# Kernel tuning notes

Hardware: AMD Instinct MI355X
Metric: run time of the kernel (lower is better)

## Reference

```python
import jax, jax.numpy as jnp
import numpy as np
import math

L, D, H, B, NT = 4, 512, 8, 128, 512
D_HID = int(D * 4.0 / 3.0)  # 682; linear0 outputs 2*D_HID for reglu
EPS = 1e-5


def layer_norm(x, g, b):
    mu = jnp.mean(x, axis=-1, keepdims=True)
    var = jnp.var(x, axis=-1, keepdims=True)
    return (x - mu) * jax.lax.rsqrt(var + EPS) * g + b


def mha(x_q, x_kv, Wq, bq, Wk, bk, Wv, bv, Wo, bo):
    q = x_q @ Wq.T + bq
    k = x_kv @ Wk.T + bk
    v = x_kv @ Wv.T + bv
    Bq, Sq, _ = q.shape
    Sk = k.shape[1]
    dh = D // H
    q = q.reshape(Bq, Sq, H, dh).transpose(0, 2, 1, 3)  # [B,H,Sq,dh]
    k = k.reshape(Bq, Sk, H, dh).transpose(0, 2, 1, 3)
    v = v.reshape(Bq, Sk, H, dh).transpose(0, 2, 1, 3)
    dots = jnp.einsum('bhqd,bhkd->bhqk', q, k) / math.sqrt(dh)
    attn = jax.nn.softmax(dots, axis=-1)
    o = jnp.einsum('bhqk,bhkd->bhqd', attn, v)
    o = o.transpose(0, 2, 1, 3).reshape(Bq, Sq, D)
    return o @ Wo.T + bo


def reglu(x):
    a, b = jnp.split(x, 2, axis=-1)
    return a * jax.nn.relu(b)


def setup_inputs() -> dict:
    key = jax.random.key(0)
    ks = iter(jax.random.split(key, 32))
    s = 0.02
    return {
        'x_num': jax.random.normal(next(ks), (B, NT, D), jnp.float32),
        'cls_w': jax.random.normal(next(ks), (1, D), jnp.float32) * s,
        'Wq': jax.random.normal(next(ks), (L, D, D), jnp.float32) * s,
        'bq': jnp.zeros((L, D), jnp.float32),
        'Wk': jax.random.normal(next(ks), (L, D, D), jnp.float32) * s,
        'bk': jnp.zeros((L, D), jnp.float32),
        'Wv': jax.random.normal(next(ks), (L, D, D), jnp.float32) * s,
        'bv': jnp.zeros((L, D), jnp.float32),
        'Wo': jax.random.normal(next(ks), (L, D, D), jnp.float32) * s,
        'bo': jnp.zeros((L, D), jnp.float32),
        'l0_w': jax.random.normal(next(ks), (L, 2 * D_HID, D), jnp.float32) * s,
        'l0_b': jnp.zeros((L, 2 * D_HID), jnp.float32),
        'l1_w': jax.random.normal(next(ks), (L, D, D_HID), jnp.float32) * s,
        'l1_b': jnp.zeros((L, D), jnp.float32),
        'n0_g': jnp.ones((L - 1, D), jnp.float32),
        'n0_b': jnp.zeros((L - 1, D), jnp.float32),
        'n1_g': jnp.ones((L, D), jnp.float32),
        'n1_b': jnp.zeros((L, D), jnp.float32),
        'ln_g': jnp.ones((D,), jnp.float32),
        'ln_b': jnp.zeros((D,), jnp.float32),
        'head_w': jax.random.normal(next(ks), (1, D), jnp.float32) * s,
        'head_b': jnp.zeros((1,), jnp.float32),
    }


def reference(x_num, cls_w, Wq, bq, Wk, bk, Wv, bv, Wo, bo,
              l0_w, l0_b, l1_w, l1_b, n0_g, n0_b, n1_g, n1_b,
              ln_g, ln_b, head_w, head_b):
    # prepend CLS token: cls_weight broadcast over batch
    x_cls = jnp.broadcast_to(cls_w[None], (x_num.shape[0], 1, D))
    x = jnp.concatenate([x_cls, x_num], axis=1)  # [B, NT+1, D]
    for i in range(L):
        is_last = i + 1 == L
        # attention block (prenormalization; layer 0 has no norm0)
        xr = layer_norm(x, n0_g[i - 1], n0_b[i - 1]) if i > 0 else x
        x_q = xr[:, :1] if is_last else xr  # last layer: query only CLS
        xr = mha(x_q, xr, Wq[i], bq[i], Wk[i], bk[i], Wv[i], bv[i], Wo[i], bo[i])
        if is_last:
            x = x[:, :1]
        x = x + xr
        # FFN block with reglu
        xr = layer_norm(x, n1_g[i], n1_b[i])
        xr = reglu(xr @ l0_w[i].T + l0_b[i])
        xr = xr @ l1_w[i].T + l1_b[i]
        x = x + xr
    x = x[:, 0]  # CLS representation [B, D]
    x = layer_norm(x, ln_g, ln_b)
    x = jax.nn.relu(x)
    x = x @ head_w.T + head_b
    return x.squeeze(-1)  # [B]
```

## Files before the change

### kernel.cpp

```cpp
#include <hip/hip_runtime.h>
#include <stdint.h>

typedef __attribute__((ext_vector_type(4))) float f32x4;
typedef __attribute__((ext_vector_type(8))) short short8;
typedef __attribute__((ext_vector_type(8))) _Float16 half8;

#define DMODEL 512
#define SEQ 513
#define BATCH 128
#define NROWS (BATCH*SEQ)
#define DHID 682
#define DHID2 1364
#define HP 768
#define QKVS 1536
#define KVB 64
#define NKT 9
#define QSF 0.1803368801111244f

__device__ __forceinline__ float h2f(ushort u){ return (float)__builtin_bit_cast(_Float16, u); }
__device__ __forceinline__ ushort f2h(float f){ return __builtin_bit_cast(ushort, (_Float16)f); }
__device__ __forceinline__ uint pk2h(float a, float b){
  return __builtin_bit_cast(uint, __builtin_amdgcn_cvt_pkrtz(a, b));
}
__device__ __forceinline__ void gload16(const void* g, void* lds){
  __builtin_amdgcn_global_load_lds((const __attribute__((address_space(1))) void*)g,
                                   (__attribute__((address_space(3))) void*)lds, 16, 0, 0);
}
__device__ __forceinline__ int xcd_wg(int orig, int nwg){
  const int q = nwg >> 3, r = nwg & 7;
  const int xcd = orig & 7, idx = orig >> 3;
  return (xcd < r) ? (xcd*(q+1) + idx) : (r*(q+1) + (xcd-r)*q + idx);
}

template<int EPI>
__global__ __launch_bounds__(256,3) void gemm_bt(
    const ushort* __restrict__ A, const ushort* __restrict__ W,
    const float* __restrict__ bias, ushort* __restrict__ Cb, float* __restrict__ Cf,
    int K, int ldc, int gx, int nwg)
{
  __shared__ char lds[32768];
  const int t = threadIdx.x, lane = t & 63, w = t >> 6;
  const int fr = lane & 15, g = lane >> 4;
  const int l7 = lane & 7, l8 = lane >> 3;
  const int wg = xcd_wg(blockIdx.x, nwg);
  const int row0 = (wg / gx) << 7;
  const int col0 = (wg % gx) << 7;
  const int wr = (w >> 1) << 6, wc = (w & 1) << 6;

  const int chunkoff = (l7 ^ l8) << 3;
  const ushort* Ag = A + (size_t)(row0 + w*8 + l8) * K + chunkoff;
  const ushort* Wg = W + (size_t)(col0 + w*8 + l8) * K + chunkoff;

  f32x4 acc[4][4] = {};

  for (int k0 = 0; k0 < K; k0 += 64) {
    __syncthreads();
#pragma unroll
    for (int p = 0; p < 4; ++p) {
      gload16(Ag + (size_t)(p*32)*K + k0, lds + p*4096 + w*1024);
      gload16(Wg + (size_t)(p*32)*K + k0, lds + 16384 + p*4096 + w*1024);
    }
    __syncthreads();
#pragma unroll
    for (int ks = 0; ks < 2; ++ks) {
      half8 af[4], wf[4];
#pragma unroll
      for (int m = 0; m < 4; ++m) {
        const int row = wr + m*16 + fr;
        af[m] = *(const half8*)(lds + row*128 + (((g + ks*4) ^ (fr & 7)) << 4));
      }
#pragma unroll
      for (int n = 0; n < 4; ++n) {
        const int row = wc + n*16 + fr;
        wf[n] = *(const half8*)(lds + 16384 + row*128 + (((g + ks*4) ^ (fr & 7)) << 4));
      }
#pragma unroll
      for (int m = 0; m < 4; ++m)
#pragma unroll
        for (int n = 0; n < 4; ++n)
          acc[m][n] = __builtin_amdgcn_mfma_f32_16x16x32_f16(af[m], wf[n], acc[m][n], 0, 0, 0);
    }
  }

  const int r0 = (lane >> 4) << 2;
#pragma unroll
  for (int m = 0; m < 4; ++m) {
    const int rg = row0 + wr + m*16 + r0;
#pragma unroll
    for (int n = 0; n < 4; ++n) {
      const int cg = col0 + wc + n*16 + fr;
      const float bi = bias[cg];
      if (EPI == 0) {
#pragma unroll
        for (int r = 0; r < 4; ++r)
          Cb[(size_t)(rg + r)*ldc + cg] = f2h(acc[m][n][r] + bi);
      } else {
#pragma unroll
        for (int r = 0; r < 4; ++r) {
          const size_t ix = (size_t)(rg + r)*ldc + cg;
          Cf[ix] += acc[m][n][r] + bi;
        }
      }
    }
  }
}

__global__ __launch_bounds__(256,2) void gemm_ffn(
    const ushort* __restrict__ A, const ushort* __restrict__ Wa, const ushort* __restrict__ Wb,
    const float* __restrict__ ba, const float* __restrict__ bb, ushort* __restrict__ H,
    int K, int ldc, int gx, int nwg)
{
  __shared__ char lds[49152];
  const int t = threadIdx.x, lane = t & 63, w = t >> 6;
  const int fr = lane & 15, g = lane >> 4;
  const int l7 = lane & 7, l8 = lane >> 3;
  const int wg = xcd_wg(blockIdx.x, nwg);
  const int row0 = (wg / gx) << 7;
  const int col0 = (wg % gx) << 7;
  const int wr = (w >> 1) << 6, wc = (w & 1) << 6;

  const int chunkoff = (l7 ^ l8) << 3;
  const ushort* Ag  = A  + (size_t)(row0 + w*8 + l8) * K + chunkoff;
  const ushort* WaG = Wa + (size_t)(col0 + w*8 + l8) * K + chunkoff;
  const ushort* WbG = Wb + (size_t)(col0 + w*8 + l8) * K + chunkoff;

  f32x4 aa[4][4] = {}, ab[4][4] = {};

  for (int k0 = 0; k0 < K; k0 += 64) {
    __syncthreads();
#pragma unroll
    for (int p = 0; p < 4; ++p) {
      gload16(Ag  + (size_t)(p*32)*K + k0, lds + p*4096 + w*1024);
      gload16(WaG + (size_t)(p*32)*K + k0, lds + 16384 + p*4096 + w*1024);
      gload16(WbG + (size_t)(p*32)*K + k0, lds + 32768 + p*4096 + w*1024);
    }
    __syncthreads();
#pragma unroll
    for (int ks = 0; ks < 2; ++ks) {
      half8 af[4], wa[4], wb[4];
#pragma unroll
      for (int m = 0; m < 4; ++m) {
        const int row = wr + m*16 + fr;
        af[m] = *(const half8*)(lds + row*128 + (((g + ks*4) ^ (fr & 7)) << 4));
      }
#pragma unroll
      for (int n = 0; n < 4; ++n) {
        const int row = wc + n*16 + fr;
        const int off = row*128 + (((g + ks*4) ^ (fr & 7)) << 4);
        wa[n] = *(const half8*)(lds + 16384 + off);
        wb[n] = *(const half8*)(lds + 32768 + off);
      }
#pragma unroll
      for (int m = 0; m < 4; ++m)
#pragma unroll
        for (int n = 0; n < 4; ++n) {
          aa[m][n] = __builtin_amdgcn_mfma_f32_16x16x32_f16(af[m], wa[n], aa[m][n], 0, 0, 0);
          ab[m][n] = __builtin_amdgcn_mfma_f32_16x16x32_f16(af[m], wb[n], ab[m][n], 0, 0, 0);
        }
    }
  }

  const int r0 = (lane >> 4) << 2;
#pragma unroll
  for (int m = 0; m < 4; ++m) {
    const int rg = row0 + wr + m*16 + r0;
#pragma unroll
    for (int n = 0; n < 4; ++n) {
      const int cg = col0 + wc + n*16 + fr;
      const float bav = ba[cg], bbv = bb[cg];
#pragma unroll
      for (int r = 0; r < 4; ++r) {
        const float av = aa[m][n][r] + bav;
        const float bv = ab[m][n][r] + bbv;
        H[(size_t)(rg + r)*ldc + cg] = f2h(av * fmaxf(bv, 0.f));
      }
    }
  }
}

__global__ __launch_bounds__(256,4) void attn_flash(
    const ushort* __restrict__ qkv, ushort* __restrict__ o)
{
  const int bid = blockIdx.x;
  const int sw = (bid & 7)*512 + (bid >> 3);
  const int qt = sw & 3;
  const int hb = sw >> 2;
  const int h = hb & 7, b = hb >> 3;
  const int t = threadIdx.x, lane = t & 63, w = t >> 6;
  const int fr = lane & 15, g = lane >> 4, gq4 = g << 2;
  const size_t rowB = (size_t)b * SEQ;
  const ushort* q = qkv;
  const ushort* k = qkv + 512;
  const ushort* v = qkv + 1024;

  __shared__ char lds[40960];
  char* const Ks  = lds;
  char* const Vs  = lds + 8192;
  char* const VTs = lds + 16384;
  char* const pb  = lds + 24576 + w*4096;

  const int qr0 = qt*128 + w*32;

  half8 qf[2][2];
#pragma unroll
  for (int nq = 0; nq < 2; ++nq) {
    const int qrow = qr0 + nq*16 + fr;
#pragma unroll
    for (int kk = 0; kk < 2; ++kk)
      qf[nq][kk] = *(const half8*)&q[(rowB + qrow)*QKVS + h*64 + kk*32 + g*8];
  }

  f32x4 accO[2][4] = {};
  float mrun[2] = {-1e30f, -1e30f};
  float lrun[2] = {0.f, 0.f};

  const int l8 = lane >> 3, l7 = lane & 7;
  const int chunk = l7 ^ l8;
  auto STAGE = [&](int kt2) {
#pragma unroll
    for (int i = 0; i < 2; ++i) {
      const int row = i*32 + (w<<3) + l8;
      const int keyg = min(kt2*KVB + row, 512);
      const size_t gsrc = (rowB + keyg)*QKVS + h*64 + chunk*8;
      gload16(k + gsrc, Ks + i*4096 + w*1024);
      gload16(v + gsrc, Vs + i*4096 + w*1024);
    }
  };

  const int db  = (lane & 7) | ((w & 1) << 3);
  const int kbq = l8 | ((w & 2) << 2);
  const int d0 = db << 2, key0 = kbq << 2;

  STAGE(0);

  for (int kt = 0; kt < NKT; ++kt) {
    __syncthreads();

    f32x4 sc[4][2] = {};
    __builtin_amdgcn_s_setprio(1);
#pragma unroll
    for (int kk = 0; kk < 2; ++kk) {
      half8 kf[4];
#pragma unroll
      for (int mk = 0; mk < 4; ++mk) {
        const int row = mk*16 + fr;
        kf[mk] = *(const half8*)(Ks + row*128 + ((kk*64 + g*16) ^ ((fr&7)<<4)));
      }
#pragma unroll
      for (int mk = 0; mk < 4; ++mk)
#pragma unroll
        for (int nq = 0; nq < 2; ++nq)
          sc[mk][nq] = __builtin_amdgcn_mfma_f32_16x16x32_f16(kf[mk], qf[nq][kk], sc[mk][nq], 0, 0, 0);
    }
    __builtin_amdgcn_s_setprio(0);

    {
      uint2 a[4];
#pragma unroll
      for (int i = 0; i < 4; ++i) {
        const int row = key0 + i;
        a[i] = *(const uint2*)(Vs + row*128 + ((d0*2) ^ ((row&7)<<4)));
      }
      uint2 bb[4];
      bb[0].x = (a[0].x & 0xffffu) | (a[1].x << 16);
      bb[0].y = (a[2].x & 0xffffu) | (a[3].x << 16);
      bb[1].x = (a[0].x >> 16) | (a[1].x & 0xffff0000u);
      bb[1].y = (a[2].x >> 16) | (a[3].x & 0xffff0000u);
      bb[2].x = (a[0].y & 0xffffu) | (a[1].y << 16);
      bb[2].y = (a[2].y & 0xffffu) | (a[3].y << 16);
      bb[3].x = (a[0].y >> 16) | (a[1].y & 0xffff0000u);
      bb[3].y = (a[2].y >> 16) | (a[3].y & 0xffff0000u);
#pragma unroll
      for (int j = 0; j < 4; ++j) {
        const int drow = d0 + j;
        *(uint2*)(VTs + drow*128 + ((key0*2) ^ ((drow&7)<<4))) = bb[j];
      }
    }

    if (kt == NKT-1) {
#pragma unroll
      for (int mk = 0; mk < 4; ++mk)
#pragma unroll
        for (int r = 0; r < 4; ++r)
          if (mk + gq4 + r) { sc[mk][0][r] = -1e30f; sc[mk][1][r] = -1e30f; }
    }

    __syncthreads();

    if (kt+1 < NKT) STAGE(kt+1);

    float al2[2];
    bool resc[2];
#pragma unroll
    for (int nq = 0; nq < 2; ++nq) {
      float tm = sc[0][nq][0];
#pragma unroll
      for (int mk = 0; mk < 4; ++mk)
#pragma unroll
        for (int r = 0; r < 4; ++r) tm = fmaxf(tm, sc[mk][nq][r]);
      tm = fmaxf(tm, __shfl_xor(tm, 16));
      tm = fmaxf(tm, __shfl_xor(tm, 32));
      float mref;
      if (__all(tm - mrun[nq] <= 8.f)) {
        mref = mrun[nq];
        al2[nq] = 1.f; resc[nq] = false;
      } else {
        const float mnew = fmaxf(mrun[nq], tm);
        al2[nq] = exp2f(mrun[nq] - mnew);
        mrun[nq] = mnew;
        mref = mnew;
        resc[nq] = true;
      }
      float rs = 0.f;
#pragma unroll
      for (int mk = 0; mk < 4; ++mk)
#pragma unroll
        for (int r = 0; r < 4; ++r) {
          const float pv = exp2f(sc[mk][nq][r] - mref);
          sc[mk][nq][r] = pv;
          rs += pv;
        }
      rs += __shfl_xor(rs, 16);
      rs += __shfl_xor(rs, 32);
      lrun[nq] = resc[nq] ? (lrun[nq]*al2[nq] + rs) : (lrun[nq] + rs);
      char* prow = pb + (nq*16 + fr)*128;
#pragma unroll
      for (int mk = 0; mk < 4; ++mk) {
        uint2 pk;
        pk.x = pk2h(sc[mk][nq][0], sc[mk][nq][1]);
        pk.y = pk2h(sc[mk][nq][2], sc[mk][nq][3]);
        *(uint2*)(prow + ((mk*32 + gq4*2) ^ ((fr&7)<<4))) = pk;
      }
    }

#pragma unroll
    for (int mq = 0; mq < 2; ++mq) {
      if (resc[mq]) {
#pragma unroll
        for (int r = 0; r < 4; ++r) {
          const float alr = __shfl(al2[mq], (lane & 48) | (gq4 + r));
#pragma unroll
          for (int dn = 0; dn < 4; ++dn) accO[mq][dn][r] *= alr;
        }
      }
    }

    asm volatile("" ::: "memory");

    __builtin_amdgcn_s_setprio(1);
#pragma unroll
    for (int kk2 = 0; kk2 < 2; ++kk2) {
      half8 pf[2];
#pragma unroll
      for (int mq = 0; mq < 2; ++mq)
        pf[mq] = *(const half8*)(pb + (mq*16 + fr)*128 + ((kk2*64 + g*16) ^ ((fr&7)<<4)));
      half8 vf[4];
#pragma unroll
      for (int dn = 0; dn < 4; ++dn) {
        const int row = dn*16 + fr;
        vf[dn] = *(const half8*)(VTs + row*128 + ((kk2*64 + g*16) ^ ((fr&7)<<4)));
      }
#pragma unroll
      for (int mq = 0; mq < 2; ++mq)
#pragma unroll
        for (int dn = 0; dn < 4; ++dn)
          accO[mq][dn] = __builtin_amdgcn_mfma_f32_16x16x32_f16(pf[mq], vf[dn], accO[mq][dn], 0, 0, 0);
    }
    __builtin_amdgcn_s_setprio(0);
  }

#pragma unroll
  for (int mq = 0; mq < 2; ++mq)
#pragma unroll
    for (int r = 0; r < 4; ++r) {
      const int qrow = qr0 + mq*16 + gq4 + r;
      const float ls = __shfl(lrun[mq], (lane & 48) | (gq4 + r));
      const float inv = 1.f / ls;
#pragma unroll
      for (int dn = 0; dn < 4; ++dn)
        o[(rowB + qrow)*DMODEL + h*64 + dn*16 + fr] = f2h(accO[mq][dn][r] * inv);
    }
}

__global__ __launch_bounds__(256) void attn_cls(
    const ushort* __restrict__ qbase, size_t qstride,
    const ushort* __restrict__ qkv,
    ushort* __restrict__ obase, size_t ostride)
{
  const int bh = blockIdx.x;
  const int b = bh >> 3, h = bh & 7;
  const int t = threadIdx.x;
  __shared__ float sc[SEQ];
  __shared__ float qsh[64];
  __shared__ float red[8];
  __shared__ float osum[256];
  const ushort* k = qkv + 512;
  const ushort* v = qkv + 1024;
  if (t < 64) qsh[t] = h2f(qbase[(size_t)b*qstride + h*64 + t]);
  __syncthreads();
  for (int key = t; key < SEQ; key += 256) {
    const ushort* kr = k + ((size_t)b*SEQ + key)*QKVS + h*64;
    float s = 0.f;
#pragma unroll 8
    for (int d = 0; d < 64; ++d) s += qsh[d]*h2f(kr[d]);
    sc[key] = s;
  }
  __syncthreads();
  float lm = -1e30f;
  for (int key = t; key < SEQ; key += 256) lm = fmaxf(lm, sc[key]);
#pragma unroll
  for (int mask=1; mask<64; mask<<=1) lm = fmaxf(lm, __shfl_xor(lm, mask));
  if ((t&63)==0) red[t>>6] = lm;
  __syncthreads();
  const float mx = fmaxf(fmaxf(red[0],red[1]), fmaxf(red[2],red[3]));
  float ls = 0.f;
  for (int key = t; key < SEQ; key += 256){ float pp = exp2f(sc[key]-mx); sc[key]=pp; ls += pp; }
#pragma unroll
  for (int mask=1; mask<64; mask<<=1) ls += __shfl_xor(ls, mask);
  if ((t&63)==0) red[4 + (t>>6)] = ls;
  __syncthreads();
  const float ssum = red[4]+red[5]+red[6]+red[7];
  const int d = t & 63, kc = t >> 6;
  float op = 0.f;
  for (int key = kc; key < SEQ; key += 4)
    op += sc[key] * h2f(v[((size_t)b*SEQ + key)*QKVS + h*64 + d]);
  osum[t] = op;
  __syncthreads();
  if (t < 64) {
    const float oo = (osum[t]+osum[64+t]+osum[128+t]+osum[192+t]) / ssum;
    obase[(size_t)b*ostride + h*64 + t] = f2h(oo);
  }
}

__global__ __launch_bounds__(256) void ln_kernel(
    const float* __restrict__ x, const float* __restrict__ gamma, const float* __restrict__ beta,
    ushort* __restrict__ out, int nrows)
{
  const int row = blockIdx.x*4 + (threadIdx.x >> 6);
  const int lane = threadIdx.x & 63;
  if (row >= nrows) return;
  const float* xr = x + (size_t)row*DMODEL;
  float4 a = *(const float4*)(xr + lane*8);
  float4 b = *(const float4*)(xr + lane*8 + 4);
  float s  = a.x+a.y+a.z+a.w+b.x+b.y+b.z+b.w;
  float ss = a.x*a.x+a.y*a.y+a.z*a.z+a.w*a.w+b.x*b.x+b.y*b.y+b.z*b.z+b.w*b.w;
#pragma unroll
  for (int mask=1; mask<64; mask<<=1){ s += __shfl_xor(s,mask); ss += __shfl_xor(ss,mask); }
  const float mu = s*(1.f/512.f);
  const float rstd = rsqrtf(ss*(1.f/512.f) - mu*mu + 1e-5f);
  float vals[8] = {a.x,a.y,a.z,a.w,b.x,b.y,b.z,b.w};
  short8 pk;
#pragma unroll
  for (int j=0;j<8;++j){
    const int c = lane*8 + j;
    pk[j] = (short)f2h((vals[j]-mu)*rstd*gamma[c] + beta[c]);
  }
  *(short8*)(out + (size_t)row*DMODEL + lane*8) = pk;
}

__global__ void embed_kernel(const float* __restrict__ x_num, const float* __restrict__ cls_w,
                             float* __restrict__ x, ushort* __restrict__ xb)
{
  const size_t i = (size_t)blockIdx.x*256 + threadIdx.x;
  if (i >= (size_t)NROWS*128) return;
  const int row = (int)(i >> 7);
  const int c4 = ((int)(i & 127)) << 2;
  const int b = row / SEQ;
  const int s = row - b*SEQ;
  float4 val;
  if (s == 0) val = *(const float4*)(cls_w + c4);
  else        val = *(const float4*)(x_num + ((size_t)b*512 + (s-1))*512 + c4);
  *(float4*)(x + (size_t)row*DMODEL + c4) = val;
  ushort4 pk;
  pk.x = f2h(val.x); pk.y = f2h(val.y); pk.z = f2h(val.z); pk.w = f2h(val.w);
  *(ushort4*)(xb + (size_t)row*DMODEL + c4) = pk;
}

__global__ void convert_pad(const float* __restrict__ in, ushort* __restrict__ out,
                            int R, int C, int RP, int CP, int layers, float scale,
                            int r0, int srcRL, size_t ostride)
{
  const size_t i = (size_t)blockIdx.x*256 + threadIdx.x;
  const size_t per = (size_t)RP*CP;
  if (i >= per*layers) return;
  const int l = (int)(i / per);
  const int rem = (int)(i - (size_t)l*per);
  const int r = rem / CP;
  const int c = rem - r*CP;
  ushort val = 0;
  if (r < R && c < C) val = f2h(in[((size_t)l*srcRL + r0 + r)*C + c] * scale);
  out[(size_t)l*ostride + (size_t)r*CP + c] = val;
}

__global__ void build_bias(const float* __restrict__ bq, const float* __restrict__ bk,
                           const float* __restrict__ bv, const float* __restrict__ l0b,
                           float* __restrict__ fqkv, float* __restrict__ fa, float* __restrict__ fb)
{
  const int i = blockIdx.x*256 + threadIdx.x;
  if (i < 4*1536) {
    const int l = i / 1536, j = i - l*1536;
    float val;
    if (j < 512)       val = bq[l*512 + j] * QSF;
    else if (j < 1024) val = bk[l*512 + j - 512];
    else               val = bv[l*512 + j - 1024];
    fqkv[i] = val;
  }
  if (i < 4*HP) {
    const int l = i / HP, j = i - l*HP;
    fa[i] = (j < DHID) ? l0b[l*DHID2 + j] : 0.f;
    fb[i] = (j < DHID) ? l0b[l*DHID2 + DHID + j] : 0.f;
  }
}

__global__ void gather_cls(const ushort* __restrict__ xb, const float* __restrict__ x,
                           ushort* __restrict__ xq, float* __restrict__ xc)
{
  const int b = blockIdx.x, lane = threadIdx.x;
  const size_t src = (size_t)b*SEQ*DMODEL;
  *(short8*)(xq + b*DMODEL + lane*8) = *(const short8*)(xb + src + lane*8);
  *(float4*)(xc + b*DMODEL + lane*8)     = *(const float4*)(x + src + lane*8);
  *(float4*)(xc + b*DMODEL + lane*8 + 4) = *(const float4*)(x + src + lane*8 + 4);
}

__global__ void head_kernel(const float* __restrict__ xc, const float* __restrict__ g,
                            const float* __restrict__ be, const float* __restrict__ hw,
                            const float* __restrict__ hb, float* __restrict__ out)
{
  const int row = blockIdx.x;
  const int lane = threadIdx.x;
  const float* xr = xc + (size_t)row*DMODEL;
  float4 a = *(const float4*)(xr + lane*8);
  float4 b = *(const float4*)(xr + lane*8 + 4);
  float s  = a.x+a.y+a.z+a.w+b.x+b.y+b.z+b.w;
  float ss = a.x*a.x+a.y*a.y+a.z*a.z+a.w*a.w+b.x*b.x+b.y*b.y+b.z*b.z+b.w*b.w;
#pragma unroll
  for (int mask=1; mask<64; mask<<=1){ s += __shfl_xor(s,mask); ss += __shfl_xor(ss,mask); }
  const float mu = s*(1.f/512.f);
  const float rstd = rsqrtf(ss*(1.f/512.f) - mu*mu + 1e-5f);
  float vals[8] = {a.x,a.y,a.z,a.w,b.x,b.y,b.z,b.w};
  float acc = 0.f;
#pragma unroll
  for (int j=0;j<8;++j){
    const int c = lane*8 + j;
    float tv = (vals[j]-mu)*rstd*g[c] + be[c];
    acc += fmaxf(tv, 0.f) * hw[c];
  }
#pragma unroll
  for (int mask=1; mask<64; mask<<=1) acc += __shfl_xor(acc, mask);
  if (lane==0) out[row] = acc + hb[0];
}

extern "C" void kernel_launch(void* const* d_in, const int* in_sizes, int n_in,
                              void* d_out, int out_size, void* d_ws, size_t ws_size,
                              hipStream_t stream)
{
  const float* x_num = (const float*)d_in[0];
  const float* cls_w = (const float*)d_in[1];
  const float* Wq = (const float*)d_in[2];
  const float* bq = (const float*)d_in[3];
  const float* Wk = (const float*)d_in[4];
  const float* bk = (const float*)d_in[5];
  const float* Wv = (const float*)d_in[6];
  const float* bv = (const float*)d_in[7];
  const float* Wo = (const float*)d_in[8];
  const float* bo = (const float*)d_in[9];
  const float* l0_w = (const float*)d_in[10];
  const float* l0_b = (const float*)d_in[11];
  const float* l1_w = (const float*)d_in[12];
  const float* l1_b = (const float*)d_in[13];
  const float* n0_g = (const float*)d_in[14];
  const float* n0_b = (const float*)d_in[15];
  const float* n1_g = (const float*)d_in[16];
  const float* n1_b = (const float*)d_in[17];
  const float* ln_g = (const float*)d_in[18];
  const float* ln_b = (const float*)d_in[19];
  const float* head_w = (const float*)d_in[20];
  const float* head_b = (const float*)d_in[21];
  float* out = (float*)d_out;

  char* p = (char*)d_ws;
  auto alloc = [&](size_t bytes){ char* r = p; p += (bytes + 255) & ~(size_t)255; return r; };

  float* x  = (float*)alloc((size_t)NROWS*DMODEL*4);
  char* U   = alloc((size_t)NROWS*DMODEL*2);
  ushort* xb = (ushort*)U;
  ushort* ob = (ushort*)U;
  char* QKVG = alloc((size_t)NROWS*QKVS*2);
  ushort* qkv = (ushort*)QKVG;
  ushort* hbuf = (ushort*)QKVG;
  ushort* wqkvb = (ushort*)alloc((size_t)4*QKVS*512*2);
  ushort* wob  = (ushort*)alloc((size_t)4*512*512*2);
  ushort* wl0a = (ushort*)alloc((size_t)4*HP*512*2);
  ushort* wl0b = (ushort*)alloc((size_t)4*HP*512*2);
  ushort* l1wp = (ushort*)alloc((size_t)4*512*HP*2);
  float*  fqkvb = (float*)alloc((size_t)4*QKVS*4);
  float*  l0ba = (float*)alloc((size_t)4*HP*4);
  float*  l0bb = (float*)alloc((size_t)4*HP*4);
  ushort* xq_cls = (ushort*)alloc(128*512*2);
  float*  xcf = (float*)alloc(128*512*4);
  ushort* qc = (ushort*)alloc(128*512*2);
  ushort* oc = (ushort*)alloc(128*512*2);
  ushort* hc = (ushort*)alloc((size_t)128*HP*2);
  ushort* xcb = (ushort*)alloc(128*512*2);

  auto cdiv = [](size_t a, size_t b){ return (unsigned)((a + b - 1)/b); };

  convert_pad<<<cdiv((size_t)4*512*512,256),256,0,stream>>>(Wq, wqkvb,            512,512,512,512,4, QSF, 0, 512, (size_t)QKVS*512);
  convert_pad<<<cdiv((size_t)4*512*512,256),256,0,stream>>>(Wk, wqkvb + 512*512,  512,512,512,512,4, 1.f, 0, 512, (size_t)QKVS*512);
  convert_pad<<<cdiv((size_t)4*512*512,256),256,0,stream>>>(Wv, wqkvb + 1024*512, 512,512,512,512,4, 1.f, 0, 512, (size_t)QKVS*512);
  convert_pad<<<cdiv((size_t)4*512*512,256),256,0,stream>>>(Wo, wob, 512,512,512,512,4, 1.f, 0, 512, (size_t)512*512);
  convert_pad<<<cdiv((size_t)4*HP*512,256),256,0,stream>>>(l0_w, wl0a, DHID,512,HP,512,4, 1.f, 0,    DHID2, (size_t)HP*512);
  convert_pad<<<cdiv((size_t)4*HP*512,256),256,0,stream>>>(l0_w, wl0b, DHID,512,HP,512,4, 1.f, DHID, DHID2, (size_t)HP*512);
  convert_pad<<<cdiv((size_t)4*512*HP,256),256,0,stream>>>(l1_w, l1wp, 512,DHID,512,HP,4, 1.f, 0, 512, (size_t)512*HP);
  build_bias<<<cdiv(4*QKVS,256),256,0,stream>>>(bq, bk, bv, l0_b, fqkvb, l0ba, l0bb);

  embed_kernel<<<cdiv((size_t)NROWS*128,256),256,0,stream>>>(x_num, cls_w, x, xb);

  const int nwQKV = 12*513, nwO = 4*513, nwF = 6*513, nwL1 = 4*513, nwKV = 8*513;
  for (int i = 0; i < 3; ++i) {
    if (i > 0)
      ln_kernel<<<cdiv(NROWS,4),256,0,stream>>>(x, n0_g+(size_t)(i-1)*512, n0_b+(size_t)(i-1)*512, xb, NROWS);
    gemm_bt<0><<<nwQKV,256,0,stream>>>(xb, wqkvb+(size_t)i*QKVS*512, fqkvb+(size_t)i*QKVS, qkv, nullptr, 512, QKVS, 12, nwQKV);
    attn_flash<<<4096,256,0,stream>>>(qkv, ob);
    attn_cls<<<1024,256,0,stream>>>(qkv + (size_t)512*QKVS, (size_t)SEQ*QKVS, qkv,
                                    ob + (size_t)512*DMODEL, (size_t)SEQ*DMODEL);
    gemm_bt<1><<<nwO,256,0,stream>>>(ob, wob+(size_t)i*262144, bo+i*512, nullptr, x, 512, 512, 4, nwO);
    ln_kernel<<<cdiv(NROWS,4),256,0,stream>>>(x, n1_g+(size_t)i*512, n1_b+(size_t)i*512, xb, NROWS);
    gemm_ffn<<<nwF,256,0,stream>>>(xb, wl0a+(size_t)i*HP*512, wl0b+(size_t)i*HP*512,
                                   l0ba+(size_t)i*HP, l0bb+(size_t)i*HP, hbuf, 512, HP, 6, nwF);
    gemm_bt<1><<<nwL1,256,0,stream>>>(hbuf, l1wp+(size_t)i*512*HP, l1_b+i*512, nullptr, x, HP, 512, 4, nwL1);
  }

  ln_kernel<<<cdiv(NROWS,4),256,0,stream>>>(x, n0_g+2*512, n0_b+2*512, xb, NROWS);
  gather_cls<<<128,64,0,stream>>>(xb, x, xq_cls, xcf);
  gemm_bt<0><<<4,256,0,stream>>>(xq_cls, wqkvb+(size_t)3*QKVS*512, fqkvb+(size_t)3*QKVS, qc, nullptr, 512, 512, 4, 4);
  gemm_bt<0><<<nwKV,256,0,stream>>>(xb, wqkvb+(size_t)3*QKVS*512 + 512*512, fqkvb+(size_t)3*QKVS + 512,
                                    qkv + 512, nullptr, 512, QKVS, 8, nwKV);
  attn_cls<<<1024,256,0,stream>>>(qc, 512, qkv, oc, 512);
  gemm_bt<1><<<4,256,0,stream>>>(oc, wob+(size_t)3*262144, bo+3*512, nullptr, xcf, 512, 512, 4, 4);
  ln_kernel<<<cdiv(128,4),256,0,stream>>>(xcf, n1_g+3*512, n1_b+3*512, xcb, 128);
  gemm_ffn<<<6,256,0,stream>>>(xcb, wl0a+(size_t)3*HP*512, wl0b+(size_t)3*HP*512,
                               l0ba+(size_t)3*HP, l0bb+(size_t)3*HP, hc, 512, HP, 6, 6);
  gemm_bt<1><<<4,256,0,stream>>>(hc, l1wp+(size_t)3*512*HP, l1_b+3*512, nullptr, xcf, HP, 512, 4, 4);
  head_kernel<<<128,64,0,stream>>>(xcf, ln_g, ln_b, head_w, head_b, out);
}
```

Measured before the change: 2.761 ms.

## Fuse output-projection GEMMs with residual add and following LayerNorm

Adds a gemm_res_ln kernel in which each block computes a full 64-row by 512-column tile, so every block owns entire rows. It adds the residual into x and then computes the row LayerNorm in-register, writing the fp16 normalized output. The kernel replaces the O-projection + ln and the L1 + ln pairs, removing separate LN passes over the whole activation. The cost is a 64-row tile with a larger LDS footprint (about 72KB), which limits occupancy, and a single-buffered loop that reloads the full weight panel every k-step.

```diff
diff --git a/kernel.cpp b/kernel.cpp
--- a/kernel.cpp
+++ b/kernel.cpp
@@ -103,6 +103,111 @@
       }
     }
   }
+}
+
+__global__ __launch_bounds__(256,2) void gemm_res_ln(
+    const ushort* __restrict__ A, const ushort* __restrict__ W,
+    const float* __restrict__ bias, float* __restrict__ x,
+    const float* __restrict__ gamma, const float* __restrict__ beta,
+    ushort* __restrict__ xb, int K)
+{
+  __shared__ char lds[73728];
+  __shared__ float red[4][64][2];
+  __shared__ float musd[64][2];
+  const int t = threadIdx.x, lane = t & 63, w = t >> 6;
+  const int fr = lane & 15, g = lane >> 4;
+  const int l7 = lane & 7, l8 = lane >> 3;
+  const int row0 = blockIdx.x << 6;
+
+  const int chunkoff = (l7 ^ l8) << 3;
+  const ushort* Ag = A + (size_t)(row0 + w*8 + l8) * K + chunkoff;
+  const ushort* Wg = W + (size_t)(w*8 + l8) * K + chunkoff;
+
+  f32x4 acc[4][8] = {};
+
+  for (int k0 = 0; k0 < K; k0 += 64) {
+    __syncthreads();
+    gload16(Ag + k0,                 lds + w*1024);
+    gload16(Ag + (size_t)32*K + k0,  lds + 4096 + w*1024);
+#pragma unroll
+    for (int p = 0; p < 16; ++p)
+      gload16(Wg + (size_t)(p*32)*K + k0, lds + 8192 + p*4096 + w*1024);
+    __syncthreads();
+#pragma unroll
+    for (int ks = 0; ks < 2; ++ks) {
+      half8 af[4], wf[8];
+#pragma unroll
+      for (int m = 0; m < 4; ++m) {
+        const int row = m*16 + fr;
+        af[m] = *(const half8*)(lds + row*128 + (((g + ks*4) ^ (fr & 7)) << 4));
+      }
+#pragma unroll
+      for (int n = 0; n < 8; ++n) {
+        const int row = (w << 7) + n*16 + fr;
+        wf[n] = *(const half8*)(lds + 8192 + row*128 + (((g + ks*4) ^ (fr & 7)) << 4));
+      }
+#pragma unroll
+      for (int m = 0; m < 4; ++m)
+#pragma unroll
+        for (int n = 0; n < 8; ++n)
+          acc[m][n] = __builtin_amdgcn_mfma_f32_16x16x32_f16(af[m], wf[n], acc[m][n], 0, 0, 0);
+    }
+  }
+
+  float ps[4][4] = {}, pss[4][4] = {};
+#pragma unroll
+  for (int n = 0; n < 8; ++n) {
+    const int cg = (w << 7) + n*16 + fr;
+    const float bi = bias[cg];
+#pragma unroll
+    for (int m = 0; m < 4; ++m) {
+#pragma unroll
+      for (int r = 0; r < 4; ++r) {
+        const size_t ix = (size_t)(row0 + m*16 + g*4 + r)*DMODEL + cg;
+        const float nv = x[ix] + acc[m][n][r] + bi;
+        x[ix] = nv;
+        acc[m][n][r] = nv;
+        ps[m][r] += nv;
+        pss[m][r] += nv*nv;
+      }
+    }
+  }
+#pragma unroll
+  for (int m = 0; m < 4; ++m)
+#pragma unroll
+    for (int r = 0; r < 4; ++r) {
+#pragma unroll
+      for (int mask = 1; mask <= 8; mask <<= 1) {
+        ps[m][r]  += __shfl_xor(ps[m][r], mask);
+        pss[m][r] += __shfl_xor(pss[m][r], mask);
+      }
+      if (fr == 0) {
+        red[w][m*16 + g*4 + r][0] = ps[m][r];
+        red[w][m*16 + g*4 + r][1] = pss[m][r];
+      }
+    }
+  __syncthreads();
+  if (t < 64) {
+    const float s  = red[0][t][0] + red[1][t][0] + red[2][t][0] + red[3][t][0];
+    const float ss = red[0][t][1] + red[1][t][1] + red[2][t][1] + red[3][t][1];
+    const float mu = s * (1.f/512.f);
+    musd[t][0] = mu;
+    musd[t][1] = rsqrtf(ss*(1.f/512.f) - mu*mu + 1e-5f);
+  }
+  __syncthreads();
+#pragma unroll
+  for (int m = 0; m < 4; ++m)
+#pragma unroll
+    for (int r = 0; r < 4; ++r) {
+      const int lrow = m*16 + g*4 + r;
+      const float mu = musd[lrow][0], rstd = musd[lrow][1];
+      const size_t rbase = (size_t)(row0 + lrow)*DMODEL;
+#pragma unroll
+      for (int n = 0; n < 8; ++n) {
+        const int cg = (w << 7) + n*16 + fr;
+        xb[rbase + cg] = f2h((acc[m][n][r] - mu)*rstd*gamma[cg] + beta[cg]);
+      }
+    }
 }
 
 __global__ __launch_bounds__(256,2) void gemm_ffn(
@@ -616,22 +721,21 @@
 
   embed_kernel<<<cdiv((size_t)NROWS*128,256),256,0,stream>>>(x_num, cls_w, x, xb);
 
-  const int nwQKV = 12*513, nwO = 4*513, nwF = 6*513, nwL1 = 4*513, nwKV = 8*513;
+  const int nwQKV = 12*513, nwF = 6*513, nwKV = 8*513;
+  const int nRL = NROWS/64;
   for (int i = 0; i < 3; ++i) {
-    if (i > 0)
-      ln_kernel<<<cdiv(NROWS,4),256,0,stream>>>(x, n0_g+(size_t)(i-1)*512, n0_b+(size_t)(i-1)*512, xb, NROWS);
     gemm_bt<0><<<nwQKV,256,0,stream>>>(xb, wqkvb+(size_t)i*QKVS*512, fqkvb+(size_t)i*QKVS, qkv, nullptr, 512, QKVS, 12, nwQKV);
     attn_flash<<<4096,256,0,stream>>>(qkv, ob);
     attn_cls<<<1024,256,0,stream>>>(qkv + (size_t)512*QKVS, (size_t)SEQ*QKVS, qkv,
                                     ob + (size_t)512*DMODEL, (size_t)SEQ*DMODEL);
-    gemm_bt<1><<<nwO,256,0,stream>>>(ob, wob+(size_t)i*262144, bo+i*512, nullptr, x, 512, 512, 4, nwO);
-    ln_kernel<<<cdiv(NROWS,4),256,0,stream>>>(x, n1_g+(size_t)i*512, n1_b+(size_t)i*512, xb, NROWS);
+    gemm_res_ln<<<nRL,256,0,stream>>>(ob, wob+(size_t)i*262144, bo+i*512, x,
+                                      n1_g+(size_t)i*512, n1_b+(size_t)i*512, xb, 512);
     gemm_ffn<<<nwF,256,0,stream>>>(xb, wl0a+(size_t)i*HP*512, wl0b+(size_t)i*HP*512,
                                    l0ba+(size_t)i*HP, l0bb+(size_t)i*HP, hbuf, 512, HP, 6, nwF);
-    gemm_bt<1><<<nwL1,256,0,stream>>>(hbuf, l1wp+(size_t)i*512*HP, l1_b+i*512, nullptr, x, HP, 512, 4, nwL1);
-  }
-
-  ln_kernel<<<cdiv(NROWS,4),256,0,stream>>>(x, n0_g+2*512, n0_b+2*512, xb, NROWS);
+    gemm_res_ln<<<nRL,256,0,stream>>>(hbuf, l1wp+(size_t)i*512*HP, l1_b+i*512, x,
+                                      n0_g+(size_t)i*512, n0_b+(size_t)i*512, xb, HP);
+  }
+
   gather_cls<<<128,64,0,stream>>>(xb, x, xq_cls, xcf);
   gemm_bt<0><<<4,256,0,stream>>>(xq_cls, wqkvb+(size_t)3*QKVS*512, fqkvb+(size_t)3*QKVS, qc, nullptr, 512, 512, 4, 4);
   gemm_bt<0><<<nwKV,256,0,stream>>>(xb, wqkvb+(size_t)3*QKVS*512 + 512*512, fqkvb+(size_t)3*QKVS + 512,
```

Result: faster. 2.650 ms (-4.0%).
